# Optimization experiments

Hardware: AMD Instinct MI355X
Metric: run time of the kernel (lower is better)

Reference implementation:

```python
import jax, jax.numpy as jnp
import numpy as np

B, H, W, C = 4, 192, 640, 32
S = 32
STEPS = np.arange(S, dtype=np.float32)  # depth steps (init kwarg 'steps')


def setup_inputs() -> dict:
    key = jax.random.key(0)
    k1, k2, k3, k4, k5 = jax.random.split(key, 5)
    x = jax.random.normal(k1, (B, H, W, C), jnp.float32)
    y = jax.random.normal(k2, (B, H, W, C), jnp.float32)
    # principal point near image center, focal ~500px, small translation T12
    origin = jnp.array([[W / 2.0, H / 2.0]], jnp.float32) + jax.random.uniform(k3, (B, 2), jnp.float32)
    focal = 500.0 + 50.0 * jax.random.uniform(k4, (B, 2), jnp.float32)
    T12 = 0.01 * jax.random.normal(k5, (B, 3), jnp.float32)
    return {"x": x, "y": y, "origin": origin, "focal": focal, "T12": T12}


def _bilinear_1img(img, sx, sy):
    # img [H,W,C]; sx [W]: source x-coord for each output column; sy [H]: source y per row.
    # Matches tf.contrib.image.transform BILINEAR with fill value 0 outside the image.
    x0 = jnp.floor(sx); fx = sx - x0
    y0 = jnp.floor(sy); fy = sy - y0
    x0i = x0.astype(jnp.int32); x1i = x0i + 1
    y0i = y0.astype(jnp.int32); y1i = y0i + 1
    mx0 = ((x0i >= 0) & (x0i < W)).astype(img.dtype)
    mx1 = ((x1i >= 0) & (x1i < W)).astype(img.dtype)
    my0 = ((y0i >= 0) & (y0i < H)).astype(img.dtype)
    my1 = ((y1i >= 0) & (y1i < H)).astype(img.dtype)
    # interpolate along y first (transform is separable: x'=a*x+b, y'=a*y+c)
    r0 = img[jnp.clip(y0i, 0, H - 1)]                     # [H,W,C]
    r1 = img[jnp.clip(y1i, 0, H - 1)]                     # [H,W,C]
    rows = (my0 * (1.0 - fy))[:, None, None] * r0 + (my1 * fy)[:, None, None] * r1
    c0 = rows[:, jnp.clip(x0i, 0, W - 1)]                 # [H,W,C]
    c1 = rows[:, jnp.clip(x1i, 0, W - 1)]
    return (mx0 * (1.0 - fx))[None, :, None] * c0 + (mx1 * fx)[None, :, None] * c1


_warp = jax.vmap(lambda img, a, b, c: _bilinear_1img(
    img,
    a * jnp.arange(W, dtype=img.dtype) + b,
    a * jnp.arange(H, dtype=img.dtype) + c))


def reference(x, y, origin, focal, T12):
    tz = T12[:, 2]  # [B]

    def per_step(d):
        safe_d = jnp.where(d == 0.0, 1.0, d)
        D = jnp.where(d == 0.0, 0.0, 1.0 / (1.0 / safe_d + tz))          # [B]
        alpha = 1.0 - D * tz                                              # [B]
        beta = D * tz * origin[:, 0] + D * focal[:, 0] * T12[:, 0]        # [B]
        gamma = D * tz * origin[:, 1] + D * focal[:, 1] * T12[:, 1]       # [B]
        shifted = _warp(x, alpha, beta, gamma)                            # [B,H,W,C]
        return jnp.mean(shifted * y, axis=3)                              # [B,H,W]

    corr = jax.lax.map(jax.checkpoint(per_step), jnp.asarray(STEPS))      # [S,B,H,W]
    return jnp.transpose(corr, (1, 2, 3, 0))                              # [B,H,W,S]
```

## Files before the change

kernel.cpp:

```cpp
#include <hip/hip_runtime.h>
#include <hip/hip_fp16.h>

#define BB 4
#define HH 192
#define WW 640
#define CC 32
#define SS 32
#define PXB 64
#define NWG (BB * HH * WW / PXB)
#define MAXW 140
#define PLANE (MAXW + 1)
#define PW 5

typedef _Float16 half2n __attribute__((ext_vector_type(2)));

#if defined(__has_builtin)
#if __has_builtin(__builtin_amdgcn_fdot2)
#define HAS_FDOT2 1
#endif
#endif

static __device__ __forceinline__ float fdot2_acc(__half2 a, __half2 b, float acc) {
#ifdef HAS_FDOT2
    return __builtin_amdgcn_fdot2(__builtin_bit_cast(half2n, a),
                                  __builtin_bit_cast(half2n, b), acc, false);
#else
    const float2 af = __half22float2(a);
    const float2 bf = __half22float2(b);
    return acc + af.x * bf.x + af.y * bf.y;
#endif
}

static __device__ __forceinline__ unsigned pk2(float w) {
    return (unsigned)__builtin_bit_cast(unsigned short, __float2half_rn(w)) * 0x10001u;
}

__global__ __launch_bounds__(256) void convert_x_kernel(const float* __restrict__ x,
                                                        __half* __restrict__ xh) {
    const size_t i = ((size_t)blockIdx.x * 256 + threadIdx.x) * 8;
    const float4 f0 = *(const float4*)(x + i);
    const float4 f1 = *(const float4*)(x + i + 4);
    uint4 u;
    u.x = __builtin_bit_cast(unsigned, __floats2half2_rn(f0.x, f0.y));
    u.y = __builtin_bit_cast(unsigned, __floats2half2_rn(f0.z, f0.w));
    u.z = __builtin_bit_cast(unsigned, __floats2half2_rn(f1.x, f1.y));
    u.w = __builtin_bit_cast(unsigned, __floats2half2_rn(f1.z, f1.w));
    *(uint4*)(xh + i) = u;
}

__global__ __launch_bounds__(64, 4) void corr_kernel(
    const __half* __restrict__ xh, const float* __restrict__ y,
    const float* __restrict__ origin, const float* __restrict__ focal,
    const float* __restrict__ T12, float* __restrict__ out)
{
    __shared__ uint4 sU[SS];
    __shared__ uint4 sV[SS];
    __shared__ uint4 comb[4][PLANE];

    const int lane = threadIdx.x;
    const int bid = ((int)blockIdx.x & 7) * (NWG >> 3) + ((int)blockIdx.x >> 3);

    const int p0 = bid * PXB;
    const int w0 = p0 % WW;
    const int h  = (p0 / WW) % HH;
    const int b  = p0 / (WW * HH);

    if (lane < SS) {
        const float tz = T12[b * 3 + 2];
        const float kx = tz * origin[b * 2 + 0] + focal[b * 2 + 0] * T12[b * 3 + 0];
        const float ky = tz * origin[b * 2 + 1] + focal[b * 2 + 1] * T12[b * 3 + 1];
        const float sf = (float)lane;
        const float D = sf * __builtin_amdgcn_rcpf(1.0f + sf * tz);
        const float alpha = 1.0f - D * tz;
        const float dkx = D * kx;
        const float dky = D * ky;

        const float syv = alpha * (float)h + dky;
        const float y0f = floorf(syv);
        const float fy  = syv - y0f;
        const int   y0  = (int)y0f;
        const int   y1  = y0 + 1;
        const float wy0 = (y0 >= 0 && y0 < HH) ? (1.0f - fy) : 0.0f;
        const float wy1 = (y1 >= 0 && y1 < HH) ? fy : 0.0f;
        const int   cy0 = min(max(y0, 0), HH - 1);
        const int   cy1 = min(max(y1, 0), HH - 1);

        const float sxa = alpha * (float)w0 + dkx;
        const float sxb = alpha * (float)(w0 + PXB - 1) + dkx;
        const int xlo = (int)floorf(fminf(sxa, sxb));
        const int xhi = (int)floorf(fmaxf(sxa, sxb)) + 1;
        const int width4 = (xhi - xlo + 1) * 4;

        uint4 U, V;
        U.x = __builtin_bit_cast(unsigned, alpha);
        U.y = __builtin_bit_cast(unsigned, dkx);
        U.z = (unsigned)xlo;
        U.w = (unsigned)width4;
        V.x = (unsigned)((cy0 * WW) << 6);
        V.y = (unsigned)((cy1 * WW) << 6);
        V.z = pk2(wy0);
        V.w = pk2(wy1);
        sU[lane] = U;
        sV[lane] = V;
    }

    const int pme = p0 + lane;
    __half2 yh[16];
    {
        const float4* yp = (const float4*)(y + (size_t)pme * CC);
#pragma unroll
        for (int q = 0; q < 8; ++q) {
            const float4 f = yp[q];
            yh[2 * q]     = __floats2half2_rn(f.x, f.y);
            yh[2 * q + 1] = __floats2half2_rn(f.z, f.w);
        }
    }

    const char* xbase = (const char*)(xh + (size_t)b * HH * WW * CC);
    const float pxf = (float)(w0 + lane);
    float* outp = out + (size_t)pme * SS;

    __syncthreads();

    uint4 U = sU[0];
    uint4 V = sV[0];
    {
        const int xlo    = (int)U.z;
        const int width4 = (int)U.w;
        if (width4 <= MAXW * 4) {
            const __half2 wy0h = __builtin_bit_cast(__half2, V.z);
            const __half2 wy1h = __builtin_bit_cast(__half2, V.w);
            for (int c = lane; c < width4; c += 64) {
                const int cpx = min(max(xlo + (c >> 2), 0), WW - 1);
                const unsigned po = (unsigned)((cpx << 6) + ((c & 3) << 4));
                const uint4 a  = *(const uint4*)(xbase + (size_t)(V.x + po));
                const uint4 bq = *(const uint4*)(xbase + (size_t)(V.y + po));
                uint4 o;
#pragma unroll
                for (int i = 0; i < 4; ++i) {
                    __half2 r = __hmul2(__builtin_bit_cast(__half2, (&a.x)[i]), wy0h);
                    r = __hfma2(__builtin_bit_cast(__half2, (&bq.x)[i]), wy1h, r);
                    (&o.x)[i] = __builtin_bit_cast(unsigned, r);
                }
                comb[c & 3][c >> 2] = o;
            }
            __syncthreads();
        }
    }

#pragma unroll 1
    for (int g = 0; g < 4; ++g) {
        float res[8];
#pragma unroll
        for (int j = 0; j < 8; ++j) {
            const int s = g * 8 + j;
            const float alpha  = __builtin_bit_cast(float, U.x);
            const float dkx    = __builtin_bit_cast(float, U.y);
            const int   xlo    = (int)U.z;
            const int   width4 = (int)U.w;

            const float sx  = alpha * pxf + dkx;
            const float x0f = floorf(sx);
            const float fx  = sx - x0f;
            const int   x0  = (int)x0f;
            const int   x1  = x0 + 1;
            const float wx0f = (x0 >= 0 && x0 < WW) ? (1.0f - fx) : 0.0f;
            const float wx1f = (x1 >= 0 && x1 < WW) ? fx : 0.0f;
            const __half2 wx0 = __builtin_bit_cast(__half2, pk2(wx0f));
            const __half2 wx1 = __builtin_bit_cast(__half2, pk2(wx1f));
            const int cx0 = min(max(x0, 0), WW - 1);
            const int cx1 = min(max(x1, 0), WW - 1);

            uint4 pa[PW], pb[PW];
            uint4 Un, Vn;
            int tn = 3, xlon = 0, width4n = 0;
            if (s + 1 < SS) {
                Un = sU[s + 1];
                Vn = sV[s + 1];
                xlon    = (int)Un.z;
                width4n = (int)Un.w;
                tn = (width4n <= PW * 64) ? 0 : ((width4n <= MAXW * 4) ? 1 : 2);
                if (tn == 0) {
#pragma unroll
                    for (int i = 0; i < PW; ++i) {
                        const int c  = lane + i * 64;
                        const int cc = min(c, width4n - 1);
                        const int cpx = min(max(xlon + (cc >> 2), 0), WW - 1);
                        const unsigned po = (unsigned)((cpx << 6) + ((cc & 3) << 4));
                        pa[i] = *(const uint4*)(xbase + (size_t)(Vn.x + po));
                        pb[i] = *(const uint4*)(xbase + (size_t)(Vn.y + po));
                    }
                }
            }

            float acc = 0.0f;
            if (width4 <= MAXW * 4) {
                const int wlim = (width4 >> 2) - 1;
                const int l0 = min(max(cx0 - xlo, 0), wlim);
                const int l1 = min(max(cx1 - xlo, 0), wlim);
                const uint4* b0 = &comb[0][l0];
                const uint4* b1 = &comb[0][l1];
                uint4 A[4], Bq[4];
#pragma unroll
                for (int i = 0; i < 4; ++i) {
                    A[i]  = b0[i * PLANE];
                    Bq[i] = b1[i * PLANE];
                }
#pragma unroll
                for (int i = 0; i < 4; ++i) {
#pragma unroll
                    for (int w = 0; w < 4; ++w) {
                        __half2 v = __hmul2(__builtin_bit_cast(__half2, (&A[i].x)[w]), wx0);
                        v = __hfma2(__builtin_bit_cast(__half2, (&Bq[i].x)[w]), wx1, v);
                        acc = fdot2_acc(v, yh[i * 4 + w], acc);
                    }
                }
            } else {
                const __half2 wy0h = __builtin_bit_cast(__half2, V.z);
                const __half2 wy1h = __builtin_bit_cast(__half2, V.w);
                const uint4* r0p0 = (const uint4*)(xbase + (size_t)(V.x + ((unsigned)cx0 << 6)));
                const uint4* r0p1 = (const uint4*)(xbase + (size_t)(V.x + ((unsigned)cx1 << 6)));
                const uint4* r1p0 = (const uint4*)(xbase + (size_t)(V.y + ((unsigned)cx0 << 6)));
                const uint4* r1p1 = (const uint4*)(xbase + (size_t)(V.y + ((unsigned)cx1 << 6)));
#pragma unroll
                for (int i = 0; i < 4; ++i) {
                    const uint4 a  = r0p0[i];
                    const uint4 bq = r0p1[i];
                    const uint4 c2 = r1p0[i];
                    const uint4 d  = r1p1[i];
#pragma unroll
                    for (int w = 0; w < 4; ++w) {
                        __half2 top = __hmul2(__builtin_bit_cast(__half2, (&a.x)[w]), wx0);
                        top = __hfma2(__builtin_bit_cast(__half2, (&bq.x)[w]), wx1, top);
                        __half2 bot = __hmul2(__builtin_bit_cast(__half2, (&c2.x)[w]), wx0);
                        bot = __hfma2(__builtin_bit_cast(__half2, (&d.x)[w]), wx1, bot);
                        __half2 v = __hmul2(top, wy0h);
                        v = __hfma2(bot, wy1h, v);
                        acc = fdot2_acc(v, yh[i * 4 + w], acc);
                    }
                }
            }

            if (s + 1 < SS) {
                if (tn == 0) {
                    const __half2 wy0h = __builtin_bit_cast(__half2, Vn.z);
                    const __half2 wy1h = __builtin_bit_cast(__half2, Vn.w);
#pragma unroll
                    for (int i = 0; i < PW; ++i) {
                        const int c = lane + i * 64;
                        if (c < width4n) {
                            uint4 o;
#pragma unroll
                            for (int q = 0; q < 4; ++q) {
                                __half2 r = __hmul2(__builtin_bit_cast(__half2, (&pa[i].x)[q]), wy0h);
                                r = __hfma2(__builtin_bit_cast(__half2, (&pb[i].x)[q]), wy1h, r);
                                (&o.x)[q] = __builtin_bit_cast(unsigned, r);
                            }
                            comb[c & 3][c >> 2] = o;
                        }
                    }
                    __syncthreads();
                } else if (tn == 1) {
                    const __half2 wy0h = __builtin_bit_cast(__half2, Vn.z);
                    const __half2 wy1h = __builtin_bit_cast(__half2, Vn.w);
                    for (int c = lane; c < width4n; c += 64) {
                        const int cpx = min(max(xlon + (c >> 2), 0), WW - 1);
                        const unsigned po = (unsigned)((cpx << 6) + ((c & 3) << 4));
                        const uint4 a  = *(const uint4*)(xbase + (size_t)(Vn.x + po));
                        const uint4 bq = *(const uint4*)(xbase + (size_t)(Vn.y + po));
                        uint4 o;
#pragma unroll
                        for (int q = 0; q < 4; ++q) {
                            __half2 r = __hmul2(__builtin_bit_cast(__half2, (&a.x)[q]), wy0h);
                            r = __hfma2(__builtin_bit_cast(__half2, (&bq.x)[q]), wy1h, r);
                            (&o.x)[q] = __builtin_bit_cast(unsigned, r);
                        }
                        comb[c & 3][c >> 2] = o;
                    }
                    __syncthreads();
                }
                U = Un;
                V = Vn;
            }

            res[j] = acc * (1.0f / 32.0f);
        }
        *(float4*)(outp + g * 8)     = make_float4(res[0], res[1], res[2], res[3]);
        *(float4*)(outp + g * 8 + 4) = make_float4(res[4], res[5], res[6], res[7]);
    }
}

extern "C" void kernel_launch(void* const* d_in, const int* in_sizes, int n_in,
                              void* d_out, int out_size, void* d_ws, size_t ws_size,
                              hipStream_t stream) {
    const float* x = (const float*)d_in[0];
    const float* y = (const float*)d_in[1];
    const float* origin = (const float*)d_in[2];
    const float* focal = (const float*)d_in[3];
    const float* T12 = (const float*)d_in[4];
    float* out = (float*)d_out;
    __half* xh = (__half*)d_ws;

    const int nelem = BB * HH * WW * CC;
    convert_x_kernel<<<nelem / (256 * 8), 256, 0, stream>>>(x, xh);

    corr_kernel<<<NWG, 64, 0, stream>>>(xh, y, origin, focal, T12, out);
}
```

Measured before the change: 324.5 us.

## Split depth steps across four waves per block with per-wave LDS buffers

After: 410.9 us. +26.6%, slower.

```diff
diff --git a/kernel.cpp b/kernel.cpp
--- a/kernel.cpp
+++ b/kernel.cpp
@@ -8,7 +8,9 @@
 #define SS 32
 #define PXB 64
 #define NWG (BB * HH * WW / PXB)
-#define MAXW 140
+#define NWAVE 4
+#define SPW 8
+#define MAXW 116
 #define PLANE (MAXW + 1)
 #define PW 5
 
@@ -33,6 +35,11 @@
 
 static __device__ __forceinline__ unsigned pk2(float w) {
     return (unsigned)__builtin_bit_cast(unsigned short, __float2half_rn(w)) * 0x10001u;
+}
+
+static __device__ __forceinline__ void wave_lds_fence() {
+    asm volatile("s_waitcnt lgkmcnt(0)" ::: "memory");
+    __builtin_amdgcn_sched_barrier(0);
 }
 
 __global__ __launch_bounds__(256) void convert_x_kernel(const float* __restrict__ x,
@@ -48,16 +55,19 @@
     *(uint4*)(xh + i) = u;
 }
 
-__global__ __launch_bounds__(64, 4) void corr_kernel(
+__global__ __launch_bounds__(256, 4) void corr_kernel(
     const __half* __restrict__ xh, const float* __restrict__ y,
     const float* __restrict__ origin, const float* __restrict__ focal,
     const float* __restrict__ T12, float* __restrict__ out)
 {
     __shared__ uint4 sU[SS];
     __shared__ uint4 sV[SS];
-    __shared__ uint4 comb[4][PLANE];
-
-    const int lane = threadIdx.x;
+    __shared__ uint4 comb[NWAVE][4][PLANE];
+
+    const int tid  = threadIdx.x;
+    const int lane = tid & 63;
+    const int wave = tid >> 6;
+
     const int bid = ((int)blockIdx.x & 7) * (NWG >> 3) + ((int)blockIdx.x >> 3);
 
     const int p0 = bid * PXB;
@@ -65,11 +75,11 @@
     const int h  = (p0 / WW) % HH;
     const int b  = p0 / (WW * HH);
 
-    if (lane < SS) {
+    if (tid < SS) {
         const float tz = T12[b * 3 + 2];
         const float kx = tz * origin[b * 2 + 0] + focal[b * 2 + 0] * T12[b * 3 + 0];
         const float ky = tz * origin[b * 2 + 1] + focal[b * 2 + 1] * T12[b * 3 + 1];
-        const float sf = (float)lane;
+        const float sf = (float)tid;
         const float D = sf * __builtin_amdgcn_rcpf(1.0f + sf * tz);
         const float alpha = 1.0f - D * tz;
         const float dkx = D * kx;
@@ -100,8 +110,8 @@
         V.y = (unsigned)((cy1 * WW) << 6);
         V.z = pk2(wy0);
         V.w = pk2(wy1);
-        sU[lane] = U;
-        sV[lane] = V;
+        sU[tid] = U;
+        sV[tid] = V;
     }
 
     const int pme = p0 + lane;
@@ -118,12 +128,14 @@
 
     const char* xbase = (const char*)(xh + (size_t)b * HH * WW * CC);
     const float pxf = (float)(w0 + lane);
-    float* outp = out + (size_t)pme * SS;
 
     __syncthreads();
 
-    uint4 U = sU[0];
-    uint4 V = sV[0];
+    uint4 (* const myc)[PLANE] = comb[wave];
+    const int s0 = wave * SPW;
+
+    uint4 U = sU[s0];
+    uint4 V = sV[s0];
     {
         const int xlo    = (int)U.z;
         const int width4 = (int)U.w;
@@ -142,152 +154,161 @@
                     r = __hfma2(__builtin_bit_cast(__half2, (&bq.x)[i]), wy1h, r);
                     (&o.x)[i] = __builtin_bit_cast(unsigned, r);
                 }
-                comb[c & 3][c >> 2] = o;
-            }
-            __syncthreads();
+                myc[c & 3][c >> 2] = o;
+            }
         }
     }
-
-#pragma unroll 1
-    for (int g = 0; g < 4; ++g) {
-        float res[8];
-#pragma unroll
-        for (int j = 0; j < 8; ++j) {
-            const int s = g * 8 + j;
-            const float alpha  = __builtin_bit_cast(float, U.x);
-            const float dkx    = __builtin_bit_cast(float, U.y);
-            const int   xlo    = (int)U.z;
-            const int   width4 = (int)U.w;
-
-            const float sx  = alpha * pxf + dkx;
-            const float x0f = floorf(sx);
-            const float fx  = sx - x0f;
-            const int   x0  = (int)x0f;
-            const int   x1  = x0 + 1;
-            const float wx0f = (x0 >= 0 && x0 < WW) ? (1.0f - fx) : 0.0f;
-            const float wx1f = (x1 >= 0 && x1 < WW) ? fx : 0.0f;
-            const __half2 wx0 = __builtin_bit_cast(__half2, pk2(wx0f));
-            const __half2 wx1 = __builtin_bit_cast(__half2, pk2(wx1f));
-            const int cx0 = min(max(x0, 0), WW - 1);
-            const int cx1 = min(max(x1, 0), WW - 1);
-
-            uint4 pa[PW], pb[PW];
-            uint4 Un, Vn;
-            int tn = 3, xlon = 0, width4n = 0;
-            if (s + 1 < SS) {
-                Un = sU[s + 1];
-                Vn = sV[s + 1];
-                xlon    = (int)Un.z;
-                width4n = (int)Un.w;
-                tn = (width4n <= PW * 64) ? 0 : ((width4n <= MAXW * 4) ? 1 : 2);
-                if (tn == 0) {
-#pragma unroll
-                    for (int i = 0; i < PW; ++i) {
-                        const int c  = lane + i * 64;
-                        const int cc = min(c, width4n - 1);
-                        const int cpx = min(max(xlon + (cc >> 2), 0), WW - 1);
-                        const unsigned po = (unsigned)((cpx << 6) + ((cc & 3) << 4));
-                        pa[i] = *(const uint4*)(xbase + (size_t)(Vn.x + po));
-                        pb[i] = *(const uint4*)(xbase + (size_t)(Vn.y + po));
-                    }
-                }
-            }
-
-            float acc = 0.0f;
-            if (width4 <= MAXW * 4) {
-                const int wlim = (width4 >> 2) - 1;
-                const int l0 = min(max(cx0 - xlo, 0), wlim);
-                const int l1 = min(max(cx1 - xlo, 0), wlim);
-                const uint4* b0 = &comb[0][l0];
-                const uint4* b1 = &comb[0][l1];
-                uint4 A[4], Bq[4];
-#pragma unroll
-                for (int i = 0; i < 4; ++i) {
-                    A[i]  = b0[i * PLANE];
-                    Bq[i] = b1[i * PLANE];
-                }
-#pragma unroll
-                for (int i = 0; i < 4; ++i) {
-#pragma unroll
-                    for (int w = 0; w < 4; ++w) {
-                        __half2 v = __hmul2(__builtin_bit_cast(__half2, (&A[i].x)[w]), wx0);
-                        v = __hfma2(__builtin_bit_cast(__half2, (&Bq[i].x)[w]), wx1, v);
-                        acc = fdot2_acc(v, yh[i * 4 + w], acc);
-                    }
-                }
-            } else {
-                const __half2 wy0h = __builtin_bit_cast(__half2, V.z);
-                const __half2 wy1h = __builtin_bit_cast(__half2, V.w);
-                const uint4* r0p0 = (const uint4*)(xbase + (size_t)(V.x + ((unsigned)cx0 << 6)));
-                const uint4* r0p1 = (const uint4*)(xbase + (size_t)(V.x + ((unsigned)cx1 << 6)));
-                const uint4* r1p0 = (const uint4*)(xbase + (size_t)(V.y + ((unsigned)cx0 << 6)));
-                const uint4* r1p1 = (const uint4*)(xbase + (size_t)(V.y + ((unsigned)cx1 << 6)));
-#pragma unroll
-                for (int i = 0; i < 4; ++i) {
-                    const uint4 a  = r0p0[i];
-                    const uint4 bq = r0p1[i];
-                    const uint4 c2 = r1p0[i];
-                    const uint4 d  = r1p1[i];
-#pragma unroll
-                    for (int w = 0; w < 4; ++w) {
-                        __half2 top = __hmul2(__builtin_bit_cast(__half2, (&a.x)[w]), wx0);
-                        top = __hfma2(__builtin_bit_cast(__half2, (&bq.x)[w]), wx1, top);
-                        __half2 bot = __hmul2(__builtin_bit_cast(__half2, (&c2.x)[w]), wx0);
-                        bot = __hfma2(__builtin_bit_cast(__half2, (&d.x)[w]), wx1, bot);
-                        __half2 v = __hmul2(top, wy0h);
-                        v = __hfma2(bot, wy1h, v);
-                        acc = fdot2_acc(v, yh[i * 4 + w], acc);
-                    }
-                }
-            }
-
-            if (s + 1 < SS) {
-                if (tn == 0) {
-                    const __half2 wy0h = __builtin_bit_cast(__half2, Vn.z);
-                    const __half2 wy1h = __builtin_bit_cast(__half2, Vn.w);
-#pragma unroll
-                    for (int i = 0; i < PW; ++i) {
-                        const int c = lane + i * 64;
-                        if (c < width4n) {
-                            uint4 o;
-#pragma unroll
-                            for (int q = 0; q < 4; ++q) {
-                                __half2 r = __hmul2(__builtin_bit_cast(__half2, (&pa[i].x)[q]), wy0h);
-                                r = __hfma2(__builtin_bit_cast(__half2, (&pb[i].x)[q]), wy1h, r);
-                                (&o.x)[q] = __builtin_bit_cast(unsigned, r);
-                            }
-                            comb[c & 3][c >> 2] = o;
-                        }
-                    }
-                    __syncthreads();
-                } else if (tn == 1) {
-                    const __half2 wy0h = __builtin_bit_cast(__half2, Vn.z);
-                    const __half2 wy1h = __builtin_bit_cast(__half2, Vn.w);
-                    for (int c = lane; c < width4n; c += 64) {
-                        const int cpx = min(max(xlon + (c >> 2), 0), WW - 1);
-                        const unsigned po = (unsigned)((cpx << 6) + ((c & 3) << 4));
-                        const uint4 a  = *(const uint4*)(xbase + (size_t)(Vn.x + po));
-                        const uint4 bq = *(const uint4*)(xbase + (size_t)(Vn.y + po));
+    wave_lds_fence();
+
+    float res[SPW];
+
+#pragma unroll
+    for (int j = 0; j < SPW; ++j) {
+        const int s = s0 + j;
+        const float alpha  = __builtin_bit_cast(float, U.x);
+        const float dkx    = __builtin_bit_cast(float, U.y);
+        const int   xlo    = (int)U.z;
+        const int   width4 = (int)U.w;
+
+        const float sx  = alpha * pxf + dkx;
+        const float x0f = floorf(sx);
+        const float fx  = sx - x0f;
+        const int   x0  = (int)x0f;
+        const int   x1  = x0 + 1;
+        const float wx0f = (x0 >= 0 && x0 < WW) ? (1.0f - fx) : 0.0f;
+        const float wx1f = (x1 >= 0 && x1 < WW) ? fx : 0.0f;
+        const __half2 wx0 = __builtin_bit_cast(__half2, pk2(wx0f));
+        const __half2 wx1 = __builtin_bit_cast(__half2, pk2(wx1f));
+        const int cx0 = min(max(x0, 0), WW - 1);
+        const int cx1 = min(max(x1, 0), WW - 1);
+
+        uint4 pa[PW], pb[PW];
+        uint4 Un, Vn;
+        int tn = 3, xlon = 0, width4n = 0;
+        if (j + 1 < SPW) {
+            Un = sU[s + 1];
+            Vn = sV[s + 1];
+            xlon    = (int)Un.z;
+            width4n = (int)Un.w;
+            tn = (width4n <= PW * 64) ? 0 : ((width4n <= MAXW * 4) ? 1 : 2);
+            if (tn == 0) {
+#pragma unroll
+                for (int i = 0; i < PW; ++i) {
+                    const int c  = lane + i * 64;
+                    const int cc = min(c, width4n - 1);
+                    const int cpx = min(max(xlon + (cc >> 2), 0), WW - 1);
+                    const unsigned po = (unsigned)((cpx << 6) + ((cc & 3) << 4));
+                    pa[i] = *(const uint4*)(xbase + (size_t)(Vn.x + po));
+                    pb[i] = *(const uint4*)(xbase + (size_t)(Vn.y + po));
+                }
+            }
+        }
+
+        float ac0 = 0.0f, ac1 = 0.0f, ac2 = 0.0f, ac3 = 0.0f;
+        if (width4 <= MAXW * 4) {
+            const int wlim = (width4 >> 2) - 1;
+            const int l0 = min(max(cx0 - xlo, 0), wlim);
+            const int l1 = min(max(cx1 - xlo, 0), wlim);
+            const uint4* b0 = &myc[0][l0];
+            const uint4* b1 = &myc[0][l1];
+            uint4 A[4], Bq[4];
+#pragma unroll
+            for (int i = 0; i < 4; ++i) {
+                A[i]  = b0[i * PLANE];
+                Bq[i] = b1[i * PLANE];
+            }
+#pragma unroll
+            for (int i = 0; i < 4; ++i) {
+                __half2 v0 = __hmul2(__builtin_bit_cast(__half2, A[i].x), wx0);
+                v0 = __hfma2(__builtin_bit_cast(__half2, Bq[i].x), wx1, v0);
+                ac0 = fdot2_acc(v0, yh[i * 4 + 0], ac0);
+                __half2 v1 = __hmul2(__builtin_bit_cast(__half2, A[i].y), wx0);
+                v1 = __hfma2(__builtin_bit_cast(__half2, Bq[i].y), wx1, v1);
+                ac1 = fdot2_acc(v1, yh[i * 4 + 1], ac1);
+                __half2 v2 = __hmul2(__builtin_bit_cast(__half2, A[i].z), wx0);
+                v2 = __hfma2(__builtin_bit_cast(__half2, Bq[i].z), wx1, v2);
+                ac2 = fdot2_acc(v2, yh[i * 4 + 2], ac2);
+                __half2 v3 = __hmul2(__builtin_bit_cast(__half2, A[i].w), wx0);
+                v3 = __hfma2(__builtin_bit_cast(__half2, Bq[i].w), wx1, v3);
+                ac3 = fdot2_acc(v3, yh[i * 4 + 3], ac3);
+            }
+        } else {
+            const __half2 wy0h = __builtin_bit_cast(__half2, V.z);
+            const __half2 wy1h = __builtin_bit_cast(__half2, V.w);
+            const uint4* r0p0 = (const uint4*)(xbase + (size_t)(V.x + ((unsigned)cx0 << 6)));
+            const uint4* r0p1 = (const uint4*)(xbase + (size_t)(V.x + ((unsigned)cx1 << 6)));
+            const uint4* r1p0 = (const uint4*)(xbase + (size_t)(V.y + ((unsigned)cx0 << 6)));
+            const uint4* r1p1 = (const uint4*)(xbase + (size_t)(V.y + ((unsigned)cx1 << 6)));
+#pragma unroll
+            for (int i = 0; i < 4; ++i) {
+                const uint4 a  = r0p0[i];
+                const uint4 bq = r0p1[i];
+                const uint4 c2 = r1p0[i];
+                const uint4 d  = r1p1[i];
+#pragma unroll
+                for (int w = 0; w < 4; ++w) {
+                    __half2 top = __hmul2(__builtin_bit_cast(__half2, (&a.x)[w]), wx0);
+                    top = __hfma2(__builtin_bit_cast(__half2, (&bq.x)[w]), wx1, top);
+                    __half2 bot = __hmul2(__builtin_bit_cast(__half2, (&c2.x)[w]), wx0);
+                    bot = __hfma2(__builtin_bit_cast(__half2, (&d.x)[w]), wx1, bot);
+                    __half2 v = __hmul2(top, wy0h);
+                    v = __hfma2(bot, wy1h, v);
+                    if (w == 0)      ac0 = fdot2_acc(v, yh[i * 4 + 0], ac0);
+                    else if (w == 1) ac1 = fdot2_acc(v, yh[i * 4 + 1], ac1);
+                    else if (w == 2) ac2 = fdot2_acc(v, yh[i * 4 + 2], ac2);
+                    else             ac3 = fdot2_acc(v, yh[i * 4 + 3], ac3);
+                }
+            }
+        }
+        const float acc = (ac0 + ac1) + (ac2 + ac3);
+
+        if (j + 1 < SPW) {
+            if (tn == 0) {
+                const __half2 wy0h = __builtin_bit_cast(__half2, Vn.z);
+                const __half2 wy1h = __builtin_bit_cast(__half2, Vn.w);
+#pragma unroll
+                for (int i = 0; i < PW; ++i) {
+                    const int c = lane + i * 64;
+                    if (c < width4n) {
                         uint4 o;
 #pragma unroll
                         for (int q = 0; q < 4; ++q) {
-                            __half2 r = __hmul2(__builtin_bit_cast(__half2, (&a.x)[q]), wy0h);
-                            r = __hfma2(__builtin_bit_cast(__half2, (&bq.x)[q]), wy1h, r);
+                            __half2 r = __hmul2(__builtin_bit_cast(__half2, (&pa[i].x)[q]), wy0h);
+                            r = __hfma2(__builtin_bit_cast(__half2, (&pb[i].x)[q]), wy1h, r);
                             (&o.x)[q] = __builtin_bit_cast(unsigned, r);
                         }
-                        comb[c & 3][c >> 2] = o;
+                        myc[c & 3][c >> 2] = o;
                     }
-                    __syncthreads();
-                }
-                U = Un;
-                V = Vn;
-            }
-
-            res[j] = acc * (1.0f / 32.0f);
-        }
-        *(float4*)(outp + g * 8)     = make_float4(res[0], res[1], res[2], res[3]);
-        *(float4*)(outp + g * 8 + 4) = make_float4(res[4], res[5], res[6], res[7]);
+                }
+            } else if (tn == 1) {
+                const __half2 wy0h = __builtin_bit_cast(__half2, Vn.z);
+                const __half2 wy1h = __builtin_bit_cast(__half2, Vn.w);
+                for (int c = lane; c < width4n; c += 64) {
+                    const int cpx = min(max(xlon + (c >> 2), 0), WW - 1);
+                    const unsigned po = (unsigned)((cpx << 6) + ((c & 3) << 4));
+                    const uint4 a  = *(const uint4*)(xbase + (size_t)(Vn.x + po));
+                    const uint4 bq = *(const uint4*)(xbase + (size_t)(Vn.y + po));
+                    uint4 o;
+#pragma unroll
+                    for (int q = 0; q < 4; ++q) {
+                        __half2 r = __hmul2(__builtin_bit_cast(__half2, (&a.x)[q]), wy0h);
+                        r = __hfma2(__builtin_bit_cast(__half2, (&bq.x)[q]), wy1h, r);
+                        (&o.x)[q] = __builtin_bit_cast(unsigned, r);
+                    }
+                    myc[c & 3][c >> 2] = o;
+                }
+            }
+            wave_lds_fence();
+            U = Un;
+            V = Vn;
+        }
+
+        res[j] = acc * (1.0f / 32.0f);
     }
+
+    float* outp = out + (size_t)pme * SS + s0;
+    *(float4*)(outp)     = make_float4(res[0], res[1], res[2], res[3]);
+    *(float4*)(outp + 4) = make_float4(res[4], res[5], res[6], res[7]);
 }
 
 extern "C" void kernel_launch(void* const* d_in, const int* in_sizes, int n_in,
@@ -304,5 +325,5 @@
     const int nelem = BB * HH * WW * CC;
     convert_x_kernel<<<nelem / (256 * 8), 256, 0, stream>>>(x, xh);
 
-    corr_kernel<<<NWG, 64, 0, stream>>>(xh, y, origin, focal, T12, out);
-}
+    corr_kernel<<<NWG, 256, 0, stream>>>(xh, y, origin, focal, T12, out);
+}
```
